# Optimization experiments

Measured on AMD Instinct MI355X. Metric: run time of the kernel, lower is better.

## Reference

```python
import jax, jax.numpy as jnp
import numpy as np

D_MODEL = 1024
NUM_HEADS = 16
HEAD_DIM = D_MODEL // NUM_HEADS
ROPE_THETA = 10000.0


def apply_rope(x, pos):
    # x: [B, H, S, Dh]; pos: [S] int. Interleaved-pair rotary embedding.
    d = x.shape[-1]
    inv_freq = 1.0 / (ROPE_THETA ** (jnp.arange(0, d, 2, dtype=jnp.float32) / d))  # [Dh/2]
    ang = pos.astype(jnp.float32)[:, None] * inv_freq[None, :]  # [S, Dh/2]
    cos, sin = jnp.cos(ang), jnp.sin(ang)
    x1 = x[..., 0::2]
    x2 = x[..., 1::2]
    r1 = x1 * cos - x2 * sin
    r2 = x1 * sin + x2 * cos
    return jnp.stack([r1, r2], axis=-1).reshape(x.shape)


def setup_inputs() -> dict:
    key = jax.random.key(0)
    ks = jax.random.split(key, 5)
    B, S = 4, 2048
    x = jax.random.normal(ks[0], (B, S, D_MODEL), dtype=jnp.float32)
    token_positions = jnp.arange(S, dtype=jnp.int32)
    scale = 1.0 / np.sqrt(D_MODEL)
    wq = jax.random.normal(ks[1], (D_MODEL, D_MODEL), dtype=jnp.float32) * scale
    wk = jax.random.normal(ks[2], (D_MODEL, D_MODEL), dtype=jnp.float32) * scale
    wv = jax.random.normal(ks[3], (D_MODEL, D_MODEL), dtype=jnp.float32) * scale
    wo = jax.random.normal(ks[4], (D_MODEL, D_MODEL), dtype=jnp.float32) * scale
    return {"x": x, "token_positions": token_positions, "wq": wq, "wk": wk, "wv": wv, "wo": wo}


def reference(x, token_positions, wq, wk, wv, wo):
    B, S, D = x.shape
    # Linear: einsum('d_out d_in, ... d_in -> ... d_out')
    def proj(w, t):
        return jnp.einsum('oi,bsi->bso', w, t)
    q = proj(wq, x).reshape(B, S, NUM_HEADS, HEAD_DIM).transpose(0, 2, 1, 3)  # [B,H,S,Dh]
    k = proj(wk, x).reshape(B, S, NUM_HEADS, HEAD_DIM).transpose(0, 2, 1, 3)
    v = proj(wv, x).reshape(B, S, NUM_HEADS, HEAD_DIM).transpose(0, 2, 1, 3)
    q = apply_rope(q, token_positions)
    k = apply_rope(k, token_positions)
    scores = jnp.einsum('bhqd,bhkd->bhqk', q, k) / jnp.sqrt(jnp.float32(HEAD_DIM))
    causal = jnp.tril(jnp.ones((S, S), dtype=bool))  # True = keep
    scores = jnp.where(causal, scores, -jnp.inf)
    attn = jax.nn.softmax(scores, axis=-1)
    out = jnp.einsum('bhqk,bhkd->bhqd', attn, v)  # [B,H,S,Dh]
    out = out.transpose(0, 2, 1, 3).reshape(B, S, D)
    return jnp.einsum('oi,bsi->bso', wo, out)
```

## Files before the change

kernel.cpp:

```cpp
#include <hip/hip_runtime.h>
#include <hip/hip_fp16.h>

#define DM   1024
#define NH   16
#define HD   64
#define BATCH 4
#define SEQ  2048
#define MROWS (BATCH*SEQ)
#define BHSD  ((size_t)BATCH*NH*SEQ*HD)

using f32x4 = __attribute__((ext_vector_type(4))) float;
using f16x8 = __attribute__((ext_vector_type(8))) _Float16;
using f16x4 = __attribute__((ext_vector_type(4))) _Float16;
using fp16x2 = __attribute__((ext_vector_type(2))) __fp16;

__device__ __forceinline__ void gload_lds16(const void* g, void* l) {
    __builtin_amdgcn_global_load_lds(
        (const __attribute__((address_space(1))) void*)g,
        (__attribute__((address_space(3))) void*)l, 16, 0, 0);
}

__global__ __launch_bounds__(256) void f32_to_f16(const float* __restrict__ in,
                                                  _Float16* __restrict__ out, int n) {
    int i = (blockIdx.x * 256 + threadIdx.x) * 4;
    if (i >= n) return;
    float4 v = *(const float4*)(in + i);
    union { _Float16 h[4]; ushort4 u; } cv;
    cv.h[0] = (_Float16)v.x; cv.h[1] = (_Float16)v.y;
    cv.h[2] = (_Float16)v.z; cv.h[3] = (_Float16)v.w;
    *(ushort4*)(out + i) = cv.u;
}

__global__ __launch_bounds__(256) void rope_table(const int* __restrict__ pos,
                                                  float2* __restrict__ tab) {
    int idx = blockIdx.x * 256 + threadIdx.x;
    int s = idx >> 5, j = idx & 31;
    float p = (float)pos[s];
    float invf = powf(10000.0f, -(float)j / 32.0f);
    float ang = p * invf;
    tab[idx] = make_float2(cosf(ang), sinf(ang));
}

template<int MODE>
__global__ __launch_bounds__(256)
void gemm_f16(const _Float16* __restrict__ A, const _Float16* __restrict__ Bw,
              float* __restrict__ outF, _Float16* __restrict__ qkv,
              const float2* __restrict__ rope) {
    __shared__ __align__(16) _Float16 lds[2][2][128][32];
    const int tid  = threadIdx.x;
    const int lane = tid & 63;
    const int wid  = tid >> 6;
    const int m0 = blockIdx.x * 128;
    const int n0 = blockIdx.y * 128;
    const int wm = (wid >> 1) * 64;
    const int wn = (wid & 1) * 64;
    const int g   = lane >> 4;
    const int r16 = lane & 15;

    const int srow0 = (wid*2 + 0)*16 + (lane >> 2);
    const int srow1 = (wid*2 + 1)*16 + (lane >> 2);
    const int sch0 = (lane & 3) ^ ((srow0 >> 1) & 3);
    const int sch1 = (lane & 3) ^ ((srow1 >> 1) & 3);
    const _Float16* Asrc0 = A  + (size_t)(m0 + srow0)*DM + sch0*8;
    const _Float16* Asrc1 = A  + (size_t)(m0 + srow1)*DM + sch1*8;
    const _Float16* Bsrc0 = Bw + (size_t)(n0 + srow0)*DM + sch0*8;
    const _Float16* Bsrc1 = Bw + (size_t)(n0 + srow1)*DM + sch1*8;

    f32x4 acc[4][4] = {};

    #define STAGE(buf, kt) do {                                           \
        const int koff = (kt)*32;                                         \
        _Float16* bA = &lds[(buf)][0][0][0];                              \
        _Float16* bB = &lds[(buf)][1][0][0];                              \
        gload_lds16(Asrc0 + koff, bA + (wid*2 + 0)*512);                  \
        gload_lds16(Asrc1 + koff, bA + (wid*2 + 1)*512);                  \
        gload_lds16(Bsrc0 + koff, bB + (wid*2 + 0)*512);                  \
        gload_lds16(Bsrc1 + koff, bB + (wid*2 + 1)*512);                  \
    } while (0)

    STAGE(0, 0);
    for (int kt = 0; kt < 32; ++kt) {
        __syncthreads();
        if (kt + 1 < 32) STAGE((kt + 1) & 1, kt + 1);
        const int buf = kt & 1;
        f16x8 af[4], bf[4];
        #pragma unroll
        for (int i = 0; i < 4; ++i) {
            int rowa = wm + i*16 + r16;
            af[i] = *(const f16x8*)&lds[buf][0][rowa][(g ^ ((rowa >> 1) & 3)) * 8];
            int rowb = wn + i*16 + r16;
            bf[i] = *(const f16x8*)&lds[buf][1][rowb][(g ^ ((rowb >> 1) & 3)) * 8];
        }
        #pragma unroll
        for (int i = 0; i < 4; ++i)
            #pragma unroll
            for (int j = 0; j < 4; ++j)
                acc[i][j] = __builtin_amdgcn_mfma_f32_16x16x32_f16(af[i], bf[j], acc[i][j], 0, 0, 0);
    }
    #undef STAGE

    #pragma unroll
    for (int i = 0; i < 4; ++i) {
        #pragma unroll
        for (int j = 0; j < 4; ++j) {
            if constexpr (MODE == 0) {
                #pragma unroll
                for (int r = 0; r < 4; ++r) {
                    const int m = m0 + wm + i*16 + g*4 + r;
                    const int n = n0 + wn + j*16 + r16;
                    outF[(size_t)m*DM + n] = acc[i][j][r];
                }
            } else {
                const int n = n0 + wn + j*16 + r16;
                const int sel = n >> 10;
                const int cc = n & 1023;
                const int h = cc >> 6, dd = cc & 63;
                if (sel == 2) {
                    const int mb = m0 + wm + i*16 + g*4;
                    const int s0 = mb & (SEQ - 1), b = mb >> 11;
                    f16x4 pk;
                    #pragma unroll
                    for (int r = 0; r < 4; ++r) pk[r] = (_Float16)acc[i][j][r];
                    *(f16x4*)(qkv + 2*BHSD + ((size_t)((b*NH + h)*HD + dd))*SEQ + s0) = pk;
                } else {
                    #pragma unroll
                    for (int r = 0; r < 4; ++r) {
                        const int m = m0 + wm + i*16 + g*4 + r;
                        float v = acc[i][j][r];
                        float vp = __shfl_xor(v, 1);
                        const int s = m & (SEQ - 1), b = m >> 11;
                        float2 cs = rope[(s << 5) + (dd >> 1)];
                        float o;
                        if (dd & 1) o = vp * cs.y + v * cs.x;
                        else        o = v * cs.x - vp * cs.y;
                        if (sel == 0) o *= 0.18033688f;
                        qkv[(size_t)sel*BHSD + ((size_t)((b*NH + h)*SEQ + s))*HD + dd] = (_Float16)o;
                    }
                }
            }
        }
    }
}

__device__ __forceinline__ void process_tile(
    const _Float16 (*__restrict__ Klb)[64], const _Float16 (*__restrict__ Vlb)[64],
    const f16x8 (&qf)[2][2], f32x4 (&ot)[2][4], float (&m)[2], float (&l)[2],
    const int Rq, const int kv0, const int g, const int r16, const int permLo) {

    f32x4 sT[2][4] = {};
    const int kchunkBase = r16 & 7;
    __builtin_amdgcn_s_setprio(1);
    #pragma unroll
    for (int ks = 0; ks < 2; ++ks) {
        f16x8 kf[4];
        #pragma unroll
        for (int n = 0; n < 4; ++n)
            kf[n] = *(const f16x8*)&Klb[n*16 + r16][(((ks<<2)|g) ^ kchunkBase)*8];
        #pragma unroll
        for (int qi = 0; qi < 2; ++qi)
            #pragma unroll
            for (int n = 0; n < 4; ++n)
                sT[qi][n] = __builtin_amdgcn_mfma_f32_16x16x32_f16(kf[n], qf[qi][ks], sT[qi][n], 0, 0, 0);
    }
    __builtin_amdgcn_s_setprio(0);

    uint breg[2][2][4];
    #pragma unroll
    for (int qi = 0; qi < 2; ++qi) {
        const bool full = (kv0 + 63 <= Rq + qi*16);
        float sv[16];
        if (full) {
            #pragma unroll
            for (int n = 0; n < 4; ++n)
                #pragma unroll
                for (int r = 0; r < 4; ++r) sv[n*4 + r] = sT[qi][n][r];
        } else {
            const int q = Rq + qi*16 + r16;
            #pragma unroll
            for (int n = 0; n < 4; ++n)
                #pragma unroll
                for (int r = 0; r < 4; ++r)
                    sv[n*4 + r] = (kv0 + n*16 + g*4 + r <= q) ? sT[qi][n][r] : -INFINITY;
        }
        float mx = sv[0];
        #pragma unroll
        for (int i = 1; i < 16; ++i) mx = fmaxf(mx, sv[i]);
        mx = fmaxf(mx, __shfl_xor(mx, 16));
        mx = fmaxf(mx, __shfl_xor(mx, 32));
        const bool need = (mx > m[qi] + 8.f);
        if (__any(need)) {
            float mnew = need ? mx : m[qi];
            float al = exp2f(m[qi] - mnew);
            m[qi] = mnew;
            l[qi] *= al;
            #pragma unroll
            for (int n = 0; n < 4; ++n) ot[qi][n] *= al;
        }
        float ps = 0.f;
        #pragma unroll
        for (int i = 0; i < 16; ++i) { sv[i] = exp2f(sv[i] - m[qi]); ps += sv[i]; }
        ps += __shfl_xor(ps, 16);
        ps += __shfl_xor(ps, 32);
        l[qi] += ps;

        uint pku[4][2];
        #pragma unroll
        for (int t = 0; t < 4; ++t)
            #pragma unroll
            for (int rp = 0; rp < 2; ++rp) {
                union { fp16x2 h; uint u; } cv;
                cv.h = __builtin_amdgcn_cvt_pkrtz(sv[t*4 + 2*rp], sv[t*4 + 2*rp + 1]);
                pku[t][rp] = cv.u;
            }
        #pragma unroll
        for (int ks = 0; ks < 2; ++ks)
            #pragma unroll
            for (int j2 = 0; j2 < 4; ++j2) {
                int src = permLo + ((j2 >> 1) << 4);
                int lo = __shfl((int)pku[2*ks    ][j2 & 1], src);
                int hi = __shfl((int)pku[2*ks + 1][j2 & 1], src);
                breg[qi][ks][j2] = (uint)((g & 2) ? hi : lo);
            }
    }

    __builtin_amdgcn_s_setprio(1);
    #pragma unroll
    for (int ks = 0; ks < 2; ++ks) {
        f16x8 vf[4];
        #pragma unroll
        for (int n = 0; n < 4; ++n)
            vf[n] = *(const f16x8*)&Vlb[n*16 + r16][(((ks<<2)|g) ^ kchunkBase)*8];
        #pragma unroll
        for (int qi = 0; qi < 2; ++qi) {
            union { uint u[4]; f16x8 h; } pb;
            #pragma unroll
            for (int j2 = 0; j2 < 4; ++j2) pb.u[j2] = breg[qi][ks][j2];
            #pragma unroll
            for (int n = 0; n < 4; ++n)
                ot[qi][n] = __builtin_amdgcn_mfma_f32_16x16x32_f16(vf[n], pb.h, ot[qi][n], 0, 0, 0);
        }
    }
    __builtin_amdgcn_s_setprio(0);
}

__global__ __launch_bounds__(256, 2)
void attn_kernel(const _Float16* __restrict__ qkv, _Float16* __restrict__ ao) {
    const int tid = threadIdx.x, lane = tid & 63, w = tid >> 6;
    const int g = lane >> 4, r16 = lane & 15;
    const int bh = blockIdx.x;
    const int jq = blockIdx.y;
    const int q0h = (15 - jq) * 128, q0l = jq * 128;
    const _Float16* Q   = qkv + (size_t)bh * SEQ * HD;
    const _Float16* Kp  = qkv + BHSD + (size_t)bh * SEQ * HD;
    const _Float16* Vpt = qkv + 2*BHSD + (size_t)bh * SEQ * HD;

    __shared__ __align__(16) _Float16 Kl[2][64][64];
    __shared__ __align__(16) _Float16 Vl[2][64][64];

    const int rA = tid >> 3,        rB = 32 + (tid >> 3);
    const int lcA = (tid & 7) ^ (rA & 7), lcB = (tid & 7) ^ (rB & 7);
    const _Float16* KsrcA = Kp  + (size_t)rA*HD + lcA*8;
    const _Float16* KsrcB = Kp  + (size_t)rB*HD + lcB*8;
    const _Float16* VsrcA = Vpt + (size_t)rA*SEQ + lcA*8;
    const _Float16* VsrcB = Vpt + (size_t)rB*SEQ + lcB*8;

    const int Rh = q0h + w*32, Rl = q0l + w*32;
    f16x8 qfh[2][2], qfl[2][2];
    #pragma unroll
    for (int qi = 0; qi < 2; ++qi)
        #pragma unroll
        for (int ks = 0; ks < 2; ++ks) {
            qfh[qi][ks] = *(const f16x8*)(Q + (size_t)(Rh + qi*16 + r16)*HD + ks*32 + g*8);
            qfl[qi][ks] = *(const f16x8*)(Q + (size_t)(Rl + qi*16 + r16)*HD + ks*32 + g*8);
        }

    f32x4 oth[2][4] = {}, otl[2][4] = {};
    float mh[2] = {-INFINITY, -INFINITY}, lh[2] = {0.f, 0.f};
    float ml[2] = {-INFINITY, -INFINITY}, ll[2] = {0.f, 0.f};

    const int nth = (q0h >> 6) + 2;
    const int ntl = (q0l >> 6) + 2;
    const int permLo = r16 + 32*(g & 1);

    #define STAGE(buf, kv0) do {                                              \
        gload_lds16(KsrcA + (size_t)(kv0)*HD, &Kl[(buf)][0][0] + tid*8);      \
        gload_lds16(KsrcB + (size_t)(kv0)*HD, &Kl[(buf)][0][0] + (256+tid)*8);\
        gload_lds16(VsrcA + (kv0),            &Vl[(buf)][0][0] + tid*8);      \
        gload_lds16(VsrcB + (kv0),            &Vl[(buf)][0][0] + (256+tid)*8);\
    } while (0)

    STAGE(0, 0);
    for (int kt = 0; kt < nth; ++kt) {
        const int kv0 = kt << 6;
        __syncthreads();
        if (kt + 1 < nth) STAGE((kt + 1) & 1, (kt + 1) << 6);
        const int buf = kt & 1;

        if (kv0 <= Rh + 31)
            process_tile(Kl[buf], Vl[buf], qfh, oth, mh, lh, Rh, kv0, g, r16, permLo);
        if (kt < ntl && kv0 <= Rl + 31)
            process_tile(Kl[buf], Vl[buf], qfl, otl, ml, ll, Rl, kv0, g, r16, permLo);
    }
    #undef STAGE

    const int b = bh >> 4, h = bh & 15;
    #pragma unroll
    for (int qi = 0; qi < 2; ++qi) {
        float invh = 1.0f / lh[qi], invl = 1.0f / ll[qi];
        const int srh = Rh + qi*16 + r16, srl = Rl + qi*16 + r16;
        _Float16* dsth = ao + ((size_t)(b*SEQ + srh))*DM + h*HD + g*4;
        _Float16* dstl = ao + ((size_t)(b*SEQ + srl))*DM + h*HD + g*4;
        #pragma unroll
        for (int n = 0; n < 4; ++n) {
            f16x4 pkh, pkl;
            #pragma unroll
            for (int r = 0; r < 4; ++r) {
                pkh[r] = (_Float16)(oth[qi][n][r] * invh);
                pkl[r] = (_Float16)(otl[qi][n][r] * invl);
            }
            *(f16x4*)(dsth + n*16) = pkh;
            *(f16x4*)(dstl + n*16) = pkl;
        }
    }
}

extern "C" void kernel_launch(void* const* d_in, const int* in_sizes, int n_in,
                              void* d_out, int out_size, void* d_ws, size_t ws_size,
                              hipStream_t stream) {
    const float* x  = (const float*)d_in[0];
    const int*   tp = (const int*)d_in[1];
    const float* wq = (const float*)d_in[2];
    const float* wk = (const float*)d_in[3];
    const float* wv = (const float*)d_in[4];
    const float* wo = (const float*)d_in[5];
    float* out = (float*)d_out;

    char* ws = (char*)d_ws;
    _Float16* xh  = (_Float16*)(ws);
    _Float16* whq = (_Float16*)(ws + 16777216);
    _Float16* woh = (_Float16*)(ws + 23068672);
    _Float16* qkv = (_Float16*)(ws + 25165824);
    _Float16* ao  = (_Float16*)(ws + 75497472);
    float2*   rope= (float2*)  (ws + 92274688);

    f32_to_f16<<<MROWS*DM/1024, 256, 0, stream>>>(x, xh, MROWS*DM);
    f32_to_f16<<<DM*DM/1024, 256, 0, stream>>>(wq, whq,            DM*DM);
    f32_to_f16<<<DM*DM/1024, 256, 0, stream>>>(wk, whq + DM*DM,    DM*DM);
    f32_to_f16<<<DM*DM/1024, 256, 0, stream>>>(wv, whq + 2*DM*DM,  DM*DM);
    f32_to_f16<<<DM*DM/1024, 256, 0, stream>>>(wo, woh,            DM*DM);
    rope_table<<<SEQ*32/256, 256, 0, stream>>>(tp, rope);

    gemm_f16<1><<<dim3(MROWS/128, 3*DM/128), 256, 0, stream>>>(xh, whq, nullptr, qkv, rope);
    attn_kernel<<<dim3(BATCH*NH, SEQ/256), 256, 0, stream>>>(qkv, ao);
    gemm_f16<0><<<dim3(MROWS/128, DM/128), 256, 0, stream>>>(ao, woh, out, nullptr, nullptr);
}
```

Baseline: 227.1 us.

## Shrink attention query tile per wave to 16 rows and double block count

```diff
diff --git a/kernel.cpp b/kernel.cpp
--- a/kernel.cpp
+++ b/kernel.cpp
@@ -144,112 +144,100 @@
 
 __device__ __forceinline__ void process_tile(
     const _Float16 (*__restrict__ Klb)[64], const _Float16 (*__restrict__ Vlb)[64],
-    const f16x8 (&qf)[2][2], f32x4 (&ot)[2][4], float (&m)[2], float (&l)[2],
+    const f16x8 (&qf)[2], f32x4 (&ot)[4], float &m, float &l,
     const int Rq, const int kv0, const int g, const int r16, const int permLo) {
 
-    f32x4 sT[2][4] = {};
+    f32x4 sT[4] = {};
     const int kchunkBase = r16 & 7;
     __builtin_amdgcn_s_setprio(1);
     #pragma unroll
     for (int ks = 0; ks < 2; ++ks) {
-        f16x8 kf[4];
+        #pragma unroll
+        for (int n = 0; n < 4; ++n) {
+            f16x8 kf = *(const f16x8*)&Klb[n*16 + r16][(((ks<<2)|g) ^ kchunkBase)*8];
+            sT[n] = __builtin_amdgcn_mfma_f32_16x16x32_f16(kf, qf[ks], sT[n], 0, 0, 0);
+        }
+    }
+    __builtin_amdgcn_s_setprio(0);
+
+    const bool full = (kv0 + 63 <= Rq);
+    float sv[16];
+    if (full) {
         #pragma unroll
         for (int n = 0; n < 4; ++n)
-            kf[n] = *(const f16x8*)&Klb[n*16 + r16][(((ks<<2)|g) ^ kchunkBase)*8];
-        #pragma unroll
-        for (int qi = 0; qi < 2; ++qi)
             #pragma unroll
-            for (int n = 0; n < 4; ++n)
-                sT[qi][n] = __builtin_amdgcn_mfma_f32_16x16x32_f16(kf[n], qf[qi][ks], sT[qi][n], 0, 0, 0);
+            for (int r = 0; r < 4; ++r) sv[n*4 + r] = sT[n][r];
+    } else {
+        const int q = Rq + r16;
+        #pragma unroll
+        for (int n = 0; n < 4; ++n)
+            #pragma unroll
+            for (int r = 0; r < 4; ++r)
+                sv[n*4 + r] = (kv0 + n*16 + 4*g + r <= q) ? sT[n][r] : -INFINITY;
+    }
+    float mx = sv[0];
+    #pragma unroll
+    for (int i = 1; i < 16; ++i) mx = fmaxf(mx, sv[i]);
+    mx = fmaxf(mx, __shfl_xor(mx, 16));
+    mx = fmaxf(mx, __shfl_xor(mx, 32));
+    const bool need = (mx > m + 8.f);
+    if (__any(need)) {
+        float mnew = need ? mx : m;
+        float al = exp2f(m - mnew);
+        m = mnew;
+        l *= al;
+        #pragma unroll
+        for (int n = 0; n < 4; ++n) ot[n] *= al;
+    }
+    float ps = 0.f;
+    #pragma unroll
+    for (int i = 0; i < 16; ++i) { sv[i] = exp2f(sv[i] - m); ps += sv[i]; }
+    ps += __shfl_xor(ps, 16);
+    ps += __shfl_xor(ps, 32);
+    l += ps;
+
+    uint pku[4][2];
+    #pragma unroll
+    for (int t = 0; t < 4; ++t)
+        #pragma unroll
+        for (int rp = 0; rp < 2; ++rp) {
+            union { fp16x2 h; uint u; } cv;
+            cv.h = __builtin_amdgcn_cvt_pkrtz(sv[t*4 + 2*rp], sv[t*4 + 2*rp + 1]);
+            pku[t][rp] = cv.u;
+        }
+    uint breg[2][4];
+    #pragma unroll
+    for (int ks = 0; ks < 2; ++ks)
+        #pragma unroll
+        for (int j2 = 0; j2 < 4; ++j2) {
+            int src = permLo + ((j2 >> 1) << 4);
+            int lo = __shfl((int)pku[2*ks    ][j2 & 1], src);
+            int hi = __shfl((int)pku[2*ks + 1][j2 & 1], src);
+            breg[ks][j2] = (uint)((g & 2) ? hi : lo);
+        }
+
+    __builtin_amdgcn_s_setprio(1);
+    #pragma unroll
+    for (int ks = 0; ks < 2; ++ks) {
+        union { uint u[4]; f16x8 h; } pb;
+        #pragma unroll
+        for (int j2 = 0; j2 < 4; ++j2) pb.u[j2] = breg[ks][j2];
+        #pragma unroll
+        for (int n = 0; n < 4; ++n) {
+            f16x8 vf = *(const f16x8*)&Vlb[n*16 + r16][(((ks<<2)|g) ^ kchunkBase)*8];
+            ot[n] = __builtin_amdgcn_mfma_f32_16x16x32_f16(vf, pb.h, ot[n], 0, 0, 0);
+        }
     }
     __builtin_amdgcn_s_setprio(0);
-
-    uint breg[2][2][4];
-    #pragma unroll
-    for (int qi = 0; qi < 2; ++qi) {
-        const bool full = (kv0 + 63 <= Rq + qi*16);
-        float sv[16];
-        if (full) {
-            #pragma unroll
-            for (int n = 0; n < 4; ++n)
-                #pragma unroll
-                for (int r = 0; r < 4; ++r) sv[n*4 + r] = sT[qi][n][r];
-        } else {
-            const int q = Rq + qi*16 + r16;
-            #pragma unroll
-            for (int n = 0; n < 4; ++n)
-                #pragma unroll
-                for (int r = 0; r < 4; ++r)
-                    sv[n*4 + r] = (kv0 + n*16 + g*4 + r <= q) ? sT[qi][n][r] : -INFINITY;
-        }
-        float mx = sv[0];
-        #pragma unroll
-        for (int i = 1; i < 16; ++i) mx = fmaxf(mx, sv[i]);
-        mx = fmaxf(mx, __shfl_xor(mx, 16));
-        mx = fmaxf(mx, __shfl_xor(mx, 32));
-        const bool need = (mx > m[qi] + 8.f);
-        if (__any(need)) {
-            float mnew = need ? mx : m[qi];
-            float al = exp2f(m[qi] - mnew);
-            m[qi] = mnew;
-            l[qi] *= al;
-            #pragma unroll
-            for (int n = 0; n < 4; ++n) ot[qi][n] *= al;
-        }
-        float ps = 0.f;
-        #pragma unroll
-        for (int i = 0; i < 16; ++i) { sv[i] = exp2f(sv[i] - m[qi]); ps += sv[i]; }
-        ps += __shfl_xor(ps, 16);
-        ps += __shfl_xor(ps, 32);
-        l[qi] += ps;
-
-        uint pku[4][2];
-        #pragma unroll
-        for (int t = 0; t < 4; ++t)
-            #pragma unroll
-            for (int rp = 0; rp < 2; ++rp) {
-                union { fp16x2 h; uint u; } cv;
-                cv.h = __builtin_amdgcn_cvt_pkrtz(sv[t*4 + 2*rp], sv[t*4 + 2*rp + 1]);
-                pku[t][rp] = cv.u;
-            }
-        #pragma unroll
-        for (int ks = 0; ks < 2; ++ks)
-            #pragma unroll
-            for (int j2 = 0; j2 < 4; ++j2) {
-                int src = permLo + ((j2 >> 1) << 4);
-                int lo = __shfl((int)pku[2*ks    ][j2 & 1], src);
-                int hi = __shfl((int)pku[2*ks + 1][j2 & 1], src);
-                breg[qi][ks][j2] = (uint)((g & 2) ? hi : lo);
-            }
-    }
-
-    __builtin_amdgcn_s_setprio(1);
-    #pragma unroll
-    for (int ks = 0; ks < 2; ++ks) {
-        f16x8 vf[4];
-        #pragma unroll
-        for (int n = 0; n < 4; ++n)
-            vf[n] = *(const f16x8*)&Vlb[n*16 + r16][(((ks<<2)|g) ^ kchunkBase)*8];
-        #pragma unroll
-        for (int qi = 0; qi < 2; ++qi) {
-            union { uint u[4]; f16x8 h; } pb;
-            #pragma unroll
-            for (int j2 = 0; j2 < 4; ++j2) pb.u[j2] = breg[qi][ks][j2];
-            #pragma unroll
-            for (int n = 0; n < 4; ++n)
-                ot[qi][n] = __builtin_amdgcn_mfma_f32_16x16x32_f16(vf[n], pb.h, ot[qi][n], 0, 0, 0);
-        }
-    }
-    __builtin_amdgcn_s_setprio(0);
-}
-
-__global__ __launch_bounds__(256, 2)
+}
+
+__global__ __launch_bounds__(256, 4)
 void attn_kernel(const _Float16* __restrict__ qkv, _Float16* __restrict__ ao) {
     const int tid = threadIdx.x, lane = tid & 63, w = tid >> 6;
     const int g = lane >> 4, r16 = lane & 15;
     const int bh = blockIdx.x;
     const int jq = blockIdx.y;
-    const int q0h = (15 - jq) * 128, q0l = jq * 128;
+    const int q0h = (31 - jq) * 64, q0l = jq * 64;
     const _Float16* Q   = qkv + (size_t)bh * SEQ * HD;
     const _Float16* Kp  = qkv + BHSD + (size_t)bh * SEQ * HD;
     const _Float16* Vpt = qkv + 2*BHSD + (size_t)bh * SEQ * HD;
@@ -264,22 +252,19 @@
     const _Float16* VsrcA = Vpt + (size_t)rA*SEQ + lcA*8;
     const _Float16* VsrcB = Vpt + (size_t)rB*SEQ + lcB*8;
 
-    const int Rh = q0h + w*32, Rl = q0l + w*32;
-    f16x8 qfh[2][2], qfl[2][2];
-    #pragma unroll
-    for (int qi = 0; qi < 2; ++qi)
-        #pragma unroll
-        for (int ks = 0; ks < 2; ++ks) {
-            qfh[qi][ks] = *(const f16x8*)(Q + (size_t)(Rh + qi*16 + r16)*HD + ks*32 + g*8);
-            qfl[qi][ks] = *(const f16x8*)(Q + (size_t)(Rl + qi*16 + r16)*HD + ks*32 + g*8);
-        }
-
-    f32x4 oth[2][4] = {}, otl[2][4] = {};
-    float mh[2] = {-INFINITY, -INFINITY}, lh[2] = {0.f, 0.f};
-    float ml[2] = {-INFINITY, -INFINITY}, ll[2] = {0.f, 0.f};
-
-    const int nth = (q0h >> 6) + 2;
-    const int ntl = (q0l >> 6) + 2;
+    const int Rh = q0h + w*16, Rl = q0l + w*16;
+    f16x8 qfh[2], qfl[2];
+    #pragma unroll
+    for (int ks = 0; ks < 2; ++ks) {
+        qfh[ks] = *(const f16x8*)(Q + (size_t)(Rh + r16)*HD + ks*32 + g*8);
+        qfl[ks] = *(const f16x8*)(Q + (size_t)(Rl + r16)*HD + ks*32 + g*8);
+    }
+
+    f32x4 oth[4] = {}, otl[4] = {};
+    float mh = -INFINITY, lh = 0.f, ml_ = -INFINITY, ll_ = 0.f;
+
+    const int nth = (q0h >> 6) + 1;
+    const int ntl = (q0l >> 6) + 1;
     const int permLo = r16 + 32*(g & 1);
 
     #define STAGE(buf, kv0) do {                                              \
@@ -296,31 +281,27 @@
         if (kt + 1 < nth) STAGE((kt + 1) & 1, (kt + 1) << 6);
         const int buf = kt & 1;
 
-        if (kv0 <= Rh + 31)
+        if (kv0 <= Rh + 15)
             process_tile(Kl[buf], Vl[buf], qfh, oth, mh, lh, Rh, kv0, g, r16, permLo);
-        if (kt < ntl && kv0 <= Rl + 31)
-            process_tile(Kl[buf], Vl[buf], qfl, otl, ml, ll, Rl, kv0, g, r16, permLo);
+        if (kt < ntl)
+            process_tile(Kl[buf], Vl[buf], qfl, otl, ml_, ll_, Rl, kv0, g, r16, permLo);
     }
     #undef STAGE
 
     const int b = bh >> 4, h = bh & 15;
-    #pragma unroll
-    for (int qi = 0; qi < 2; ++qi) {
-        float invh = 1.0f / lh[qi], invl = 1.0f / ll[qi];
-        const int srh = Rh + qi*16 + r16, srl = Rl + qi*16 + r16;
-        _Float16* dsth = ao + ((size_t)(b*SEQ + srh))*DM + h*HD + g*4;
-        _Float16* dstl = ao + ((size_t)(b*SEQ + srl))*DM + h*HD + g*4;
-        #pragma unroll
-        for (int n = 0; n < 4; ++n) {
-            f16x4 pkh, pkl;
-            #pragma unroll
-            for (int r = 0; r < 4; ++r) {
-                pkh[r] = (_Float16)(oth[qi][n][r] * invh);
-                pkl[r] = (_Float16)(otl[qi][n][r] * invl);
-            }
-            *(f16x4*)(dsth + n*16) = pkh;
-            *(f16x4*)(dstl + n*16) = pkl;
-        }
+    const float invh = 1.0f / lh, invl = 1.0f / ll_;
+    _Float16* dsth = ao + ((size_t)(b*SEQ + Rh + r16))*DM + h*HD + g*4;
+    _Float16* dstl = ao + ((size_t)(b*SEQ + Rl + r16))*DM + h*HD + g*4;
+    #pragma unroll
+    for (int n = 0; n < 4; ++n) {
+        f16x4 pkh, pkl;
+        #pragma unroll
+        for (int r = 0; r < 4; ++r) {
+            pkh[r] = (_Float16)(oth[n][r] * invh);
+            pkl[r] = (_Float16)(otl[n][r] * invl);
+        }
+        *(f16x4*)(dsth + n*16) = pkh;
+        *(f16x4*)(dstl + n*16) = pkl;
     }
 }
 
@@ -351,6 +332,6 @@
     rope_table<<<SEQ*32/256, 256, 0, stream>>>(tp, rope);
 
     gemm_f16<1><<<dim3(MROWS/128, 3*DM/128), 256, 0, stream>>>(xh, whq, nullptr, qkv, rope);
-    attn_kernel<<<dim3(BATCH*NH, SEQ/256), 256, 0, stream>>>(qkv, ao);
+    attn_kernel<<<dim3(BATCH*NH, 16), 256, 0, stream>>>(qkv, ao);
     gemm_f16<0><<<dim3(MROWS/128, DM/128), 256, 0, stream>>>(ao, woh, out, nullptr, nullptr);
 }
```

Measured after the change: 223.0 us. Within noise of the previous version (-1.8%).
